# Performance work log

Measured on AMD Instinct MI355X. Metric: run time of the kernel, lower is better.

Reference implementation:

```python
import jax, jax.numpy as jnp
import numpy as np

H, W = 1024, 1024        # heatmap resolution
C = 128                  # n_targets (clusters)
N_ITER = 8               # n_iterations


def setup_inputs() -> dict:
    key = jax.random.key(0)
    k1, k2 = jax.random.split(key)
    # clusters live in pixel coordinate space [0,H) x [0,W)
    clusters = jax.random.uniform(k1, (C, 2), dtype=jnp.float32) * jnp.array([H, W], dtype=jnp.float32)
    heatmap = jax.random.uniform(k2, (H, W), dtype=jnp.float32)
    return {"clusters": clusters, "heatmap": heatmap}


def reference(clusters, heatmap):
    # pixel coordinate grid [H, W, 2] with (row, col) ordering, matching
    # clusters[c,0]-row, clusters[c,1]-col in the original code
    rows = jnp.arange(H, dtype=jnp.float32)
    cols = jnp.arange(W, dtype=jnp.float32)
    coords = jnp.stack(jnp.meshgrid(rows, cols, indexing='ij'), axis=-1)  # [H, W, 2]

    def step(cs, _):
        # Euclidean distance from every pixel to every cluster, clamped to >= 1
        diff = coords[:, :, None, :] - cs[None, None, :, :]          # [H, W, C, 2]
        dist = jnp.maximum(1.0, jnp.sqrt(jnp.sum(diff * diff, axis=-1)))  # [H, W, C]
        assign = jnp.argmin(dist, axis=-1)                            # [H, W] nearest cluster
        best_dist = jnp.min(dist, axis=-1)                            # [H, W]
        # weighted scatter-add of pixel coords into their nearest cluster
        contrib = coords * (heatmap / best_dist)[..., None]           # [H, W, 2]
        new_cs = jax.ops.segment_sum(contrib.reshape(-1, 2), assign.reshape(-1), num_segments=C)
        return new_cs.astype(jnp.float32), None

    cs, _ = jax.lax.scan(step, clusters, None, length=N_ITER)
    return cs
```

## Files before the change

kernel.cpp:

```cpp
#include <hip/hip_runtime.h>
#include <float.h>

constexpr int H = 1024, W = 1024, C = 128, N_ITER = 8;
constexpr int TPB = 256;
constexpr int TILE = 32;
constexpr int PPT = 4;
constexpr int K = 32;
constexpr int SLOTS = 2 * C;
constexpr int NBLK = (H / TILE) * (W / TILE);
constexpr int NCNT = 128;
constexpr int CNT_STRIDE = 16;
constexpr int ARRIVE_DEPTH = NBLK / NCNT;

__device__ __forceinline__ void waitVmem() {
    asm volatile("s_waitcnt vmcnt(0)" ::: "memory");
}

__device__ __forceinline__ float sum32_if(const float* base, int tid) {
    const float* p = base + tid;
    float s = 0.0f;
#pragma unroll
    for (int g = 0; g < 4; ++g) {
        const float* q = p + (size_t)g * 8 * SLOTS;
        float a0, a1, a2, a3, a4, a5, a6, a7;
        asm volatile(
            "global_load_dword %0, %8, off sc0 sc1\n\t"
            "global_load_dword %1, %9, off sc0 sc1\n\t"
            "global_load_dword %2, %10, off sc0 sc1\n\t"
            "global_load_dword %3, %11, off sc0 sc1\n\t"
            "global_load_dword %4, %12, off sc0 sc1\n\t"
            "global_load_dword %5, %13, off sc0 sc1\n\t"
            "global_load_dword %6, %14, off sc0 sc1\n\t"
            "global_load_dword %7, %15, off sc0 sc1\n\t"
            "s_waitcnt vmcnt(0)"
            : "=&v"(a0), "=&v"(a1), "=&v"(a2), "=&v"(a3),
              "=&v"(a4), "=&v"(a5), "=&v"(a6), "=&v"(a7)
            : "v"(q),            "v"(q + SLOTS),     "v"(q + 2 * SLOTS),
              "v"(q + 3 * SLOTS), "v"(q + 4 * SLOTS), "v"(q + 5 * SLOTS),
              "v"(q + 6 * SLOTS), "v"(q + 7 * SLOTS)
            : "memory");
        s = s + a0; s = s + a1; s = s + a2; s = s + a3;
        s = s + a4; s = s + a5; s = s + a6; s = s + a7;
    }
    return s;
}

__global__ __launch_bounds__(TPB) void kmeans_fused(
    const float* __restrict__ cur0,
    const float* __restrict__ heatmap,
    float* __restrict__ shards,
    int*   __restrict__ barCnt,
    int*   __restrict__ flags,
    float* __restrict__ clsPub,
    float* __restrict__ out)
{
    __shared__ float2 cls[C];
    __shared__ float2 cand[C];
    __shared__ int    candIdx[C];
    __shared__ float  waveMin[2];
    __shared__ int    waveCnt[2];
    __shared__ float  acc[SLOTS];
    __shared__ unsigned char dupf[C];

    const int tid   = threadIdx.x;
    const int bid   = blockIdx.x;
    const int tileR = (bid >> 5) * TILE;
    const int tileC = (bid & 31) * TILE;

    const int   rowIn = tid >> 3;
    const float fr    = (float)(tileR + rowIn);
    const int   col0  = tileC + (tid & 7) * PPT;
    const float4 h4   = *(const float4*)(heatmap + (size_t)(tileR + rowIn) * W + col0);
    float hval[PPT] = { h4.x, h4.y, h4.z, h4.w };
    float colf[PPT];
#pragma unroll
    for (int p = 0; p < PPT; ++p) colf[p] = (float)(col0 + p);

    for (int it = 0; it < N_ITER; ++it) {
        float coord;
        if (it == 0) {
            coord = cur0[tid];
        } else {
            const int prevIt = it - 1;
            if (bid == 0) {
                if (tid < NCNT) {
                    int* cptr = barCnt + ((size_t)prevIt * NCNT + tid) * CNT_STRIDE;
                    while (__hip_atomic_load(cptr, __ATOMIC_RELAXED,
                                             __HIP_MEMORY_SCOPE_AGENT) < ARRIVE_DEPTH)
                        __builtin_amdgcn_s_sleep(2);
                }
                __syncthreads();
                const float s = sum32_if(shards + (size_t)prevIt * K * SLOTS, tid);
                __hip_atomic_store(clsPub + (size_t)prevIt * SLOTS + tid, s,
                                   __ATOMIC_RELAXED, __HIP_MEMORY_SCOPE_AGENT);
                waitVmem();
                __syncthreads();
                if (tid == 0)
                    __hip_atomic_fetch_add(flags + (size_t)prevIt * CNT_STRIDE, 1,
                                           __ATOMIC_RELAXED, __HIP_MEMORY_SCOPE_AGENT);
                coord = s;
            } else {
                if (tid == 0) {
                    int* fptr = flags + (size_t)prevIt * CNT_STRIDE;
                    while (__hip_atomic_load(fptr, __ATOMIC_RELAXED,
                                             __HIP_MEMORY_SCOPE_AGENT) == 0)
                        __builtin_amdgcn_s_sleep(4);
                }
                __syncthreads();
                coord = __hip_atomic_load(clsPub + (size_t)prevIt * SLOTS + tid,
                                          __ATOMIC_RELAXED, __HIP_MEMORY_SCOPE_AGENT);
            }
        }

        acc[tid] = 0.0f;
        if (tid < C) dupf[tid] = 0;
        ((float*)cls)[tid] = coord;
        __syncthreads();

        const int    di  = tid & (C - 1);
        const float2 dme = cls[di];

        float dcen = 0.0f;
        if (tid < C) {
            const float dxr = dme.x - ((float)tileR + 15.5f);
            const float dyc = dme.y - ((float)tileC + 15.5f);
            dcen = sqrtf(dxr * dxr + dyc * dyc);
            float m = dcen;
#pragma unroll
            for (int off = 32; off > 0; off >>= 1)
                m = fminf(m, __shfl_xor(m, off));
            if ((tid & 63) == 0) waveMin[tid >> 6] = m;
        }

        {
            const int kLo = (tid < C) ? 1 : 33;
#pragma unroll 8
            for (int kk = 0; kk < 32; ++kk) {
                const int k = kLo + kk;
                const int j = (di + k) & (C - 1);
                const float2 o = cls[j];
                if (o.x == dme.x && o.y == dme.y)
                    dupf[(di + k < C) ? (di + k) : di] = 1;
            }
        }
        __syncthreads();

        bool keep = false;
        int  pre  = 0;
        if (tid < C) {
            const float thr = fminf(waveMin[0], waveMin[1]) + 44.84062f;
            keep = (dcen <= thr) && (dupf[tid] == 0);
            const unsigned long long mask = __ballot(keep);
            const int lane = tid & 63;
            pre = __popcll(mask & ((1ull << lane) - 1ull));
            if (lane == 0) waveCnt[tid >> 6] = __popcll(mask);
        }
        __syncthreads();
        if (keep) {
            const int pos = pre + ((tid >= 64) ? waveCnt[0] : 0);
            cand[pos]    = cls[tid];
            candIdx[pos] = tid;
        }
        __syncthreads();

        const int nCand = waveCnt[0] + waveCnt[1];

        float best[PPT];
        int   bi[PPT];
#pragma unroll
        for (int p = 0; p < PPT; ++p) { best[p] = FLT_MAX; bi[p] = 0; }

        for (int k = 0; k < nCand; ++k) {
            const float2 cl = cand[k];
            const int    ci = candIdx[k];
            const float  dx  = fr - cl.x;
            const float  dx2 = dx * dx;
#pragma unroll
            for (int p = 0; p < PPT; ++p) {
                const float dy  = colf[p] - cl.y;
                const float d2  = fmaf(dy, dy, dx2);
                const float key = fmaxf(d2, 1.0f);
                const bool  lt  = key < best[p];
                bi[p]   = lt ? ci  : bi[p];
                best[p] = lt ? key : best[p];
            }
        }

#pragma unroll
        for (int p = 0; p < PPT; ++p) {
            const float bd  = fmaxf(1.0f, sqrtf(best[p]));
            const float wgt = hval[p] / bd;
            float v0 = fr      * wgt;
            float v1 = colf[p] * wgt;
            const int b0 = __shfl(bi[p], 0);
            if (__ballot(bi[p] == b0) == 0xFFFFFFFFFFFFFFFFull) {
#pragma unroll
                for (int off = 32; off > 0; off >>= 1) {
                    v0 += __shfl_xor(v0, off);
                    v1 += __shfl_xor(v1, off);
                }
                if ((tid & 63) == 0) {
                    unsafeAtomicAdd(&acc[2 * b0 + 0], v0);
                    unsafeAtomicAdd(&acc[2 * b0 + 1], v1);
                }
            } else {
                unsafeAtomicAdd(&acc[2 * bi[p] + 0], v0);
                unsafeAtomicAdd(&acc[2 * bi[p] + 1], v1);
            }
        }
        __syncthreads();

        const float a = acc[tid];
        if (a != 0.0f)
            unsafeAtomicAdd(&shards[(size_t)it * K * SLOTS
                                    + (bid & (K - 1)) * SLOTS + tid], a);

        waitVmem();
        __syncthreads();
        if (tid == 0)
            __hip_atomic_fetch_add(
                barCnt + ((size_t)it * NCNT + (bid & (NCNT - 1))) * CNT_STRIDE, 1,
                __ATOMIC_RELAXED, __HIP_MEMORY_SCOPE_AGENT);
    }

    if (bid == 0) {
        if (tid < NCNT) {
            int* cptr = barCnt + ((size_t)(N_ITER - 1) * NCNT + tid) * CNT_STRIDE;
            while (__hip_atomic_load(cptr, __ATOMIC_RELAXED,
                                     __HIP_MEMORY_SCOPE_AGENT) < ARRIVE_DEPTH)
                __builtin_amdgcn_s_sleep(2);
        }
        __syncthreads();
        out[tid] = sum32_if(shards + (size_t)(N_ITER - 1) * K * SLOTS, tid);
    }
}

__global__ __launch_bounds__(TPB) void kmeans_step(
    const float* __restrict__ cur0,
    const float* __restrict__ prevShards,
    const float* __restrict__ heatmap,
    float* __restrict__ outShards)
{
    __shared__ float2 cls[C];
    __shared__ float2 cand[C];
    __shared__ int    candIdx[C];
    __shared__ float  waveMin[2];
    __shared__ int    waveCnt[2];
    __shared__ float  acc[SLOTS];
    __shared__ unsigned char dupf[C];

    const int tid   = threadIdx.x;
    const int tileR = (blockIdx.x >> 5) * TILE;
    const int tileC = (blockIdx.x & 31) * TILE;

    acc[tid] = 0.0f;
    if (tid < C) dupf[tid] = 0;

    float coord;
    if (prevShards) {
        float s = 0.0f;
#pragma unroll
        for (int k = 0; k < K; ++k) s += prevShards[k * SLOTS + tid];
        coord = s;
    } else {
        coord = cur0[tid];
    }
    ((float*)cls)[tid] = coord;
    __syncthreads();

    const int    di  = tid & (C - 1);
    const float2 dme = cls[di];

    float dcen = 0.0f;
    if (tid < C) {
        const float dxr = dme.x - ((float)tileR + 15.5f);
        const float dyc = dme.y - ((float)tileC + 15.5f);
        dcen = sqrtf(dxr * dxr + dyc * dyc);
        float m = dcen;
#pragma unroll
        for (int off = 32; off > 0; off >>= 1)
            m = fminf(m, __shfl_xor(m, off));
        if ((tid & 63) == 0) waveMin[tid >> 6] = m;
    }
    {
        const int kLo = (tid < C) ? 1 : 33;
#pragma unroll 8
        for (int kk = 0; kk < 32; ++kk) {
            const int k = kLo + kk;
            const int j = (di + k) & (C - 1);
            const float2 o = cls[j];
            if (o.x == dme.x && o.y == dme.y)
                dupf[(di + k < C) ? (di + k) : di] = 1;
        }
    }
    __syncthreads();

    bool keep = false;
    int  pre  = 0;
    if (tid < C) {
        const float thr = fminf(waveMin[0], waveMin[1]) + 44.84062f;
        keep = (dcen <= thr) && (dupf[tid] == 0);
        const unsigned long long mask = __ballot(keep);
        const int lane = tid & 63;
        pre = __popcll(mask & ((1ull << lane) - 1ull));
        if (lane == 0) waveCnt[tid >> 6] = __popcll(mask);
    }
    __syncthreads();
    if (keep) {
        const int pos = pre + ((tid >= 64) ? waveCnt[0] : 0);
        cand[pos]    = cls[tid];
        candIdx[pos] = tid;
    }
    __syncthreads();

    const int nCand = waveCnt[0] + waveCnt[1];

    const int   rowIn = tid >> 3;
    const float fr    = (float)(tileR + rowIn);
    const int   col0  = tileC + (tid & 7) * PPT;
    const float4 h4   = *(const float4*)(heatmap + (size_t)(tileR + rowIn) * W + col0);

    float hval[PPT] = { h4.x, h4.y, h4.z, h4.w };
    float colf[PPT], best[PPT];
    int   bi[PPT];
#pragma unroll
    for (int p = 0; p < PPT; ++p) {
        colf[p] = (float)(col0 + p);
        best[p] = FLT_MAX;
        bi[p]   = 0;
    }

    for (int k = 0; k < nCand; ++k) {
        const float2 cl = cand[k];
        const int    ci = candIdx[k];
        const float  dx  = fr - cl.x;
        const float  dx2 = dx * dx;
#pragma unroll
        for (int p = 0; p < PPT; ++p) {
            const float dy  = colf[p] - cl.y;
            const float d2  = fmaf(dy, dy, dx2);
            const float key = fmaxf(d2, 1.0f);
            const bool  lt  = key < best[p];
            bi[p]   = lt ? ci  : bi[p];
            best[p] = lt ? key : best[p];
        }
    }

#pragma unroll
    for (int p = 0; p < PPT; ++p) {
        const float bd  = fmaxf(1.0f, sqrtf(best[p]));
        const float wgt = hval[p] / bd;
        float v0 = fr      * wgt;
        float v1 = colf[p] * wgt;
        const int b0 = __shfl(bi[p], 0);
        if (__ballot(bi[p] == b0) == 0xFFFFFFFFFFFFFFFFull) {
#pragma unroll
            for (int off = 32; off > 0; off >>= 1) {
                v0 += __shfl_xor(v0, off);
                v1 += __shfl_xor(v1, off);
            }
            if ((tid & 63) == 0) {
                unsafeAtomicAdd(&acc[2 * b0 + 0], v0);
                unsafeAtomicAdd(&acc[2 * b0 + 1], v1);
            }
        } else {
            unsafeAtomicAdd(&acc[2 * bi[p] + 0], v0);
            unsafeAtomicAdd(&acc[2 * bi[p] + 1], v1);
        }
    }
    __syncthreads();

    const float a = acc[tid];
    if (a != 0.0f)
        unsafeAtomicAdd(&outShards[(blockIdx.x & (K - 1)) * SLOTS + tid], a);
}

__global__ __launch_bounds__(SLOTS) void kmeans_finalize(
    const float* __restrict__ shards,
    float* __restrict__ out)
{
    const int tid = threadIdx.x;
    float s = 0.0f;
#pragma unroll
    for (int k = 0; k < K; ++k) s += shards[k * SLOTS + tid];
    out[tid] = s;
}

extern "C" void kernel_launch(void* const* d_in, const int* in_sizes, int n_in,
                              void* d_out, int out_size, void* d_ws, size_t ws_size,
                              hipStream_t stream) {
    const float* clusters = (const float*)d_in[0];
    const float* heatmap  = (const float*)d_in[1];
    float* out = (float*)d_out;

    float* shards = (float*)d_ws;
    const size_t shardBytes = (size_t)N_ITER * K * SLOTS * sizeof(float);
    int* barCnt = (int*)((char*)d_ws + shardBytes);
    const size_t cntBytes = (size_t)N_ITER * NCNT * CNT_STRIDE * sizeof(int);
    int* flags = (int*)((char*)barCnt + cntBytes);
    const size_t flagBytes = (size_t)N_ITER * CNT_STRIDE * sizeof(int);
    float* clsPub = (float*)((char*)flags + flagBytes);
    const size_t pubBytes = (size_t)N_ITER * SLOTS * sizeof(float);

    hipMemsetAsync(d_ws, 0, shardBytes + cntBytes + flagBytes + pubBytes, stream);

    void* kargs[] = { (void*)&clusters, (void*)&heatmap, (void*)&shards,
                      (void*)&barCnt,   (void*)&flags,   (void*)&clsPub,
                      (void*)&out };
    hipError_t e = hipLaunchCooperativeKernel((const void*)kmeans_fused,
                                              dim3(NBLK), dim3(TPB),
                                              kargs, 0, stream);
    if (e != hipSuccess) {
        (void)hipGetLastError();
        const size_t perIter = (size_t)K * SLOTS;
        for (int it = 0; it < N_ITER; ++it) {
            const float* prev = (it == 0) ? nullptr : (shards + (it - 1) * perIter);
            float* dst = shards + it * perIter;
            kmeans_step<<<NBLK, TPB, 0, stream>>>(clusters, prev, heatmap, dst);
        }
        kmeans_finalize<<<1, SLOTS, 0, stream>>>(shards + (N_ITER - 1) * perIter, out);
    }
}
```

Before: 174.9 us.

## Replace flag barrier with self-validating replicated centroid publish; hoist dedup into reducer

Block 0 now runs the duplicate-centroid detection once per iteration, marks duplicates as infinity, and publishes the centroids with the sign bit flipped into 16 replicated copies. Because every encoded value is nonzero, readers can poll the data itself instead of a separate flag. Each other block polls its own replica with a wave ballot until every value is nonzero, which removes one flag round trip and spreads the polling load across 16 locations. The per-block O(C) dedup loop is dropped, launch bounds ask for 4 blocks per CU, and the inline-asm shard reduction is replaced by atomic loads. The cost is extra stores from block 0, more dedup work on the critical path in that block, and correctness depends on the nonzero encoding invariant.

Result: faster. 164.9 us (-5.7%).

```diff
diff --git a/kernel.cpp b/kernel.cpp
--- a/kernel.cpp
+++ b/kernel.cpp
@@ -11,47 +11,19 @@
 constexpr int NCNT = 128;
 constexpr int CNT_STRIDE = 16;
 constexpr int ARRIVE_DEPTH = NBLK / NCNT;
+constexpr int NREP = 16;
+constexpr unsigned SIGNB = 0x80000000u;
 
 __device__ __forceinline__ void waitVmem() {
     asm volatile("s_waitcnt vmcnt(0)" ::: "memory");
 }
 
-__device__ __forceinline__ float sum32_if(const float* base, int tid) {
-    const float* p = base + tid;
-    float s = 0.0f;
-#pragma unroll
-    for (int g = 0; g < 4; ++g) {
-        const float* q = p + (size_t)g * 8 * SLOTS;
-        float a0, a1, a2, a3, a4, a5, a6, a7;
-        asm volatile(
-            "global_load_dword %0, %8, off sc0 sc1\n\t"
-            "global_load_dword %1, %9, off sc0 sc1\n\t"
-            "global_load_dword %2, %10, off sc0 sc1\n\t"
-            "global_load_dword %3, %11, off sc0 sc1\n\t"
-            "global_load_dword %4, %12, off sc0 sc1\n\t"
-            "global_load_dword %5, %13, off sc0 sc1\n\t"
-            "global_load_dword %6, %14, off sc0 sc1\n\t"
-            "global_load_dword %7, %15, off sc0 sc1\n\t"
-            "s_waitcnt vmcnt(0)"
-            : "=&v"(a0), "=&v"(a1), "=&v"(a2), "=&v"(a3),
-              "=&v"(a4), "=&v"(a5), "=&v"(a6), "=&v"(a7)
-            : "v"(q),            "v"(q + SLOTS),     "v"(q + 2 * SLOTS),
-              "v"(q + 3 * SLOTS), "v"(q + 4 * SLOTS), "v"(q + 5 * SLOTS),
-              "v"(q + 6 * SLOTS), "v"(q + 7 * SLOTS)
-            : "memory");
-        s = s + a0; s = s + a1; s = s + a2; s = s + a3;
-        s = s + a4; s = s + a5; s = s + a6; s = s + a7;
-    }
-    return s;
-}
-
-__global__ __launch_bounds__(TPB) void kmeans_fused(
+__global__ __launch_bounds__(TPB, 4) void kmeans_fused(
     const float* __restrict__ cur0,
     const float* __restrict__ heatmap,
     float* __restrict__ shards,
     int*   __restrict__ barCnt,
-    int*   __restrict__ flags,
-    float* __restrict__ clsPub,
+    unsigned* __restrict__ clsPub,
     float* __restrict__ out)
 {
     __shared__ float2 cls[C];
@@ -90,58 +62,70 @@
                         __builtin_amdgcn_s_sleep(2);
                 }
                 __syncthreads();
-                const float s = sum32_if(shards + (size_t)prevIt * K * SLOTS, tid);
-                __hip_atomic_store(clsPub + (size_t)prevIt * SLOTS + tid, s,
-                                   __ATOMIC_RELAXED, __HIP_MEMORY_SCOPE_AGENT);
-                waitVmem();
+                const float* b = shards + (size_t)prevIt * K * SLOTS + tid;
+                float v[K];
+#pragma unroll
+                for (int k = 0; k < K; ++k)
+                    v[k] = __hip_atomic_load(b + (size_t)k * SLOTS,
+                                             __ATOMIC_RELAXED, __HIP_MEMORY_SCOPE_AGENT);
+                float s = 0.0f;
+#pragma unroll
+                for (int k = 0; k < K; ++k) s += v[k];
+
+                if (tid < C) dupf[tid] = 0;
+                ((float*)cls)[tid] = s;
                 __syncthreads();
-                if (tid == 0)
-                    __hip_atomic_fetch_add(flags + (size_t)prevIt * CNT_STRIDE, 1,
-                                           __ATOMIC_RELAXED, __HIP_MEMORY_SCOPE_AGENT);
-                coord = s;
-            } else {
-                if (tid == 0) {
-                    int* fptr = flags + (size_t)prevIt * CNT_STRIDE;
-                    while (__hip_atomic_load(fptr, __ATOMIC_RELAXED,
-                                             __HIP_MEMORY_SCOPE_AGENT) == 0)
-                        __builtin_amdgcn_s_sleep(4);
+                {
+                    const int    sdi  = tid & (C - 1);
+                    const float2 sdme = cls[sdi];
+                    const int kLo = (tid < C) ? 1 : 33;
+#pragma unroll 8
+                    for (int kk = 0; kk < 32; ++kk) {
+                        const int k = kLo + kk;
+                        const int j = (sdi + k) & (C - 1);
+                        const float2 o = cls[j];
+                        if (o.x == sdme.x && o.y == sdme.y)
+                            dupf[(sdi + k < C) ? (sdi + k) : sdi] = 1;
+                    }
                 }
                 __syncthreads();
-                coord = __hip_atomic_load(clsPub + (size_t)prevIt * SLOTS + tid,
-                                          __ATOMIC_RELAXED, __HIP_MEMORY_SCOPE_AGENT);
+                const float pv = dupf[tid >> 1] ? (float)INFINITY : s;
+                const unsigned enc = __float_as_uint(pv) ^ SIGNB;
+                unsigned* pb = clsPub + (size_t)prevIt * NREP * SLOTS;
+#pragma unroll
+                for (int r = 0; r < NREP; ++r)
+                    __hip_atomic_store(pb + r * SLOTS + tid, enc,
+                                       __ATOMIC_RELAXED, __HIP_MEMORY_SCOPE_AGENT);
+                coord = pv;
+            } else {
+                const unsigned* src = clsPub
+                    + ((size_t)prevIt * NREP + (bid & (NREP - 1))) * SLOTS;
+                unsigned u;
+                for (;;) {
+                    u = __hip_atomic_load(src + tid, __ATOMIC_RELAXED,
+                                          __HIP_MEMORY_SCOPE_AGENT);
+                    if (__ballot(u != 0u) == 0xFFFFFFFFFFFFFFFFull) break;
+                    __builtin_amdgcn_s_sleep(4);
+                }
+                coord = __uint_as_float(u ^ SIGNB);
             }
         }
 
         acc[tid] = 0.0f;
-        if (tid < C) dupf[tid] = 0;
         ((float*)cls)[tid] = coord;
         __syncthreads();
-
-        const int    di  = tid & (C - 1);
-        const float2 dme = cls[di];
 
         float dcen = 0.0f;
         if (tid < C) {
-            const float dxr = dme.x - ((float)tileR + 15.5f);
-            const float dyc = dme.y - ((float)tileC + 15.5f);
+            const float2 cl = cls[tid];
+            const float dxr = cl.x - ((float)tileR + 15.5f);
+            const float dyc = cl.y - ((float)tileC + 15.5f);
             dcen = sqrtf(dxr * dxr + dyc * dyc);
             float m = dcen;
 #pragma unroll
             for (int off = 32; off > 0; off >>= 1)
                 m = fminf(m, __shfl_xor(m, off));
             if ((tid & 63) == 0) waveMin[tid >> 6] = m;
-        }
-
-        {
-            const int kLo = (tid < C) ? 1 : 33;
-#pragma unroll 8
-            for (int kk = 0; kk < 32; ++kk) {
-                const int k = kLo + kk;
-                const int j = (di + k) & (C - 1);
-                const float2 o = cls[j];
-                if (o.x == dme.x && o.y == dme.y)
-                    dupf[(di + k < C) ? (di + k) : di] = 1;
-            }
         }
         __syncthreads();
 
@@ -149,7 +133,7 @@
         int  pre  = 0;
         if (tid < C) {
             const float thr = fminf(waveMin[0], waveMin[1]) + 44.84062f;
-            keep = (dcen <= thr) && (dupf[tid] == 0);
+            keep = (dcen <= thr);
             const unsigned long long mask = __ballot(keep);
             const int lane = tid & 63;
             pre = __popcll(mask & ((1ull << lane) - 1ull));
@@ -231,7 +215,16 @@
                 __builtin_amdgcn_s_sleep(2);
         }
         __syncthreads();
-        out[tid] = sum32_if(shards + (size_t)(N_ITER - 1) * K * SLOTS, tid);
+        const float* b = shards + (size_t)(N_ITER - 1) * K * SLOTS + tid;
+        float v[K];
+#pragma unroll
+        for (int k = 0; k < K; ++k)
+            v[k] = __hip_atomic_load(b + (size_t)k * SLOTS,
+                                     __ATOMIC_RELAXED, __HIP_MEMORY_SCOPE_AGENT);
+        float s = 0.0f;
+#pragma unroll
+        for (int k = 0; k < K; ++k) s += v[k];
+        out[tid] = s;
     }
 }
 
@@ -397,16 +390,13 @@
     const size_t shardBytes = (size_t)N_ITER * K * SLOTS * sizeof(float);
     int* barCnt = (int*)((char*)d_ws + shardBytes);
     const size_t cntBytes = (size_t)N_ITER * NCNT * CNT_STRIDE * sizeof(int);
-    int* flags = (int*)((char*)barCnt + cntBytes);
-    const size_t flagBytes = (size_t)N_ITER * CNT_STRIDE * sizeof(int);
-    float* clsPub = (float*)((char*)flags + flagBytes);
-    const size_t pubBytes = (size_t)N_ITER * SLOTS * sizeof(float);
-
-    hipMemsetAsync(d_ws, 0, shardBytes + cntBytes + flagBytes + pubBytes, stream);
+    unsigned* clsPub = (unsigned*)((char*)barCnt + cntBytes);
+    const size_t pubBytes = (size_t)N_ITER * NREP * SLOTS * sizeof(unsigned);
+
+    hipMemsetAsync(d_ws, 0, shardBytes + cntBytes + pubBytes, stream);
 
     void* kargs[] = { (void*)&clusters, (void*)&heatmap, (void*)&shards,
-                      (void*)&barCnt,   (void*)&flags,   (void*)&clsPub,
-                      (void*)&out };
+                      (void*)&barCnt,   (void*)&clsPub,  (void*)&out };
     hipError_t e = hipLaunchCooperativeKernel((const void*)kmeans_fused,
                                               dim3(NBLK), dim3(TPB),
                                               kargs, 0, stream);
```
